# Optimization experiments

Hardware: AMD Instinct MI355X
Metric: run time of the kernel (lower is better)

## Reference

```python
import jax, jax.numpy as jnp
import numpy as np

HEADS = 8

def setup_inputs() -> dict:
    key = jax.random.key(0)
    k1, k2, k3, k4 = jax.random.split(key, 4)
    B, C_IN, H, W = 16, 256, 64, 64
    C_OUT = 256
    s = 1.0 / np.sqrt(C_IN)
    x = jax.random.normal(k1, (B, C_IN, H, W), dtype=jnp.float32)
    wq = jax.random.normal(k2, (C_OUT, C_IN), dtype=jnp.float32) * s
    wk = jax.random.normal(k3, (C_OUT, C_IN), dtype=jnp.float32) * s
    wv = jax.random.normal(k4, (C_OUT, C_IN), dtype=jnp.float32) * s
    return {"x": x, "wq": wq, "wk": wk, "wv": wv}

def _feat(t):
    # ELU(x) + 1  (positive feature map for linear attention)
    return jax.nn.elu(t) + 1.0

def reference(x, wq, wk, wv):
    B, C, H, W = x.shape
    M = H * W
    c_out = wq.shape[0]
    dh = c_out // HEADS
    scale = 1.0 / np.sqrt(dh)
    xf = x.reshape(B, C, M)  # flatten spatial
    # 1x1 conv (no bias) == channel matmul; reshape to [B, heads, dh, M]
    def proj(w):
        return jnp.einsum('oc,bcm->bom', w, xf).reshape(B, HEADS, dh, M)
    q = _feat(proj(wq)) * scale
    k = _feat(proj(wk)) * scale
    v = proj(wv)
    # linear attention: KV = k v^T over spatial, then apply to q
    KV = jnp.einsum('bhcm,bhdm->bhcd', k, v)          # [B,h,dh,dh]
    out = jnp.einsum('bhcd,bhcm->bhdm', KV, q)        # [B,h,dh,M]
    k_sum = k.sum(axis=-1)                             # [B,h,dh]
    denom = jnp.einsum('bhcm,bhc->bhm', q, k_sum)      # [B,h,M]
    denom = jnp.maximum(denom, 1e-6)[:, :, None, :]
    out = out / denom
    return out.reshape(B, c_out, H, W)
```

## Files before the change

### kernel.cpp

```cpp
#include <hip/hip_runtime.h>
#include <hip/hip_bf16.h>


typedef __attribute__((ext_vector_type(8))) short bf16x8;
typedef __attribute__((ext_vector_type(4))) float f32x4;
typedef __attribute__((ext_vector_type(4))) unsigned int u32x4;
typedef __attribute__((ext_vector_type(4))) float float4v;

#define DEVI static __device__ __forceinline__

DEVI unsigned short f2bf(float f){
  unsigned int u = __builtin_bit_cast(unsigned int, f);
  u = (u + 0x7fffu + ((u >> 16) & 1u)) >> 16;
  return (unsigned short)u;
}
DEVI unsigned int pk2(float a, float b){
  return (unsigned int)f2bf(a) | ((unsigned int)f2bf(b) << 16);
}
DEVI float feat(float p){
  return (p > 0.f ? p + 1.f : __expf(p)) * 0.17677669529663687f;
}

DEVI f32x4 mfma16(u32x4 a, u32x4 b, f32x4 c){
  return __builtin_amdgcn_mfma_f32_16x16x32_bf16(
      __builtin_bit_cast(bf16x8, a), __builtin_bit_cast(bf16x8, b), c, 0, 0, 0);
}

DEVI int swz8(int m){ return ((m ^ (m >> 3)) & 7) << 4; }

typedef __attribute__((address_space(3))) unsigned int as3_u32;
typedef __attribute__((address_space(1))) const unsigned int as1_u32;
DEVI void gload16(const void* g, void* l){
  __builtin_amdgcn_global_load_lds((as1_u32*)g, (as3_u32*)l, 16, 0, 0);
}
DEVI void stage_tile(const char* src, void* buf, int w, int lane){
  #pragma unroll
  for (int i = 0; i < 4; ++i){
    int ub = w * 1024 + i * 8192;
    gload16(src + ub + lane * 16, (char*)buf + ub);
  }
}

DEVI void stage_load(const float* __restrict__ xb, int m0, int tid, float4v* r){
  #pragma unroll
  for (int it = 0; it < 2; ++it){
    int cq = (tid >> 4) + it * 32;
    int mq = tid & 15;
    const float* p = xb + (size_t)(cq * 4) * 4096 + m0 + mq * 4;
    r[it*4+0] = *(const float4v*)(p);
    r[it*4+1] = *(const float4v*)(p + 4096);
    r[it*4+2] = *(const float4v*)(p + 8192);
    r[it*4+3] = *(const float4v*)(p + 12288);
  }
}
DEVI void stage_write(unsigned short* xT, int tid, const float4v* r){
  #pragma unroll
  for (int it = 0; it < 2; ++it){
    int cq = (tid >> 4) + it * 32;
    int mq = tid & 15;
    int c0 = cq * 4, ml0 = mq * 4;
    #pragma unroll
    for (int j = 0; j < 4; ++j){
      int m = ml0 + j;
      unsigned int lo = pk2(r[it*4+0][j], r[it*4+1][j]);
      unsigned int hi = pk2(r[it*4+2][j], r[it*4+3][j]);
      int off = m * 512 + ((c0 * 2) ^ swz8(m));
      unsigned long long v = (unsigned long long)lo | ((unsigned long long)hi << 32);
      *(unsigned long long*)((char*)xT + off) = v;
    }
  }
}

__global__ void wconv(const float* __restrict__ wq, const float* __restrict__ wk,
                      const float* __restrict__ wv,
                      unsigned short* __restrict__ wkvf, unsigned short* __restrict__ wqf){
  int t = blockIdx.x * 256 + threadIdx.x;
  if (t < 16384){
    int lane = t & 63, kk = (t >> 6) & 7, ot = (t >> 9) & 3, h = t >> 11;
    int l15 = lane & 15, hi = lane >> 4;
    const float* src = (ot < 2) ? (wk + (size_t)(h * 32 + ot * 16 + l15) * 256)
                                : (wv + (size_t)(h * 32 + (ot - 2) * 16 + l15) * 256);
    src += kk * 32 + hi * 8;
    unsigned short* dst = wkvf + (size_t)t * 8;
    #pragma unroll
    for (int j = 0; j < 8; ++j) dst[j] = f2bf(src[j]);
  } else if (t < 24576){
    int u = t - 16384;
    int lane = u & 63, kk = (u >> 6) & 7, ot = (u >> 9) & 1, h = u >> 10;
    int l15 = lane & 15, hi = lane >> 4;
    const float* src = wq + (size_t)(h * 32 + ot * 16 + l15) * 256 + kk * 32 + hi * 8;
    unsigned short* dst = wqf + (size_t)u * 8;
    #pragma unroll
    for (int j = 0; j < 8; ++j) dst[j] = f2bf(src[j]);
  }
}

__global__ void __launch_bounds__(512) xcvt(const float* __restrict__ x,
                                            unsigned short* __restrict__ ximg){
  __shared__ __align__(16) unsigned short xT[16384];
  const int tid = threadIdx.x;
  const int ch = blockIdx.x, b = blockIdx.y;
  const float* xb = x + (size_t)b * (256 * 4096);
  for (int sub = 0; sub < 2; ++sub){
    int m0 = ch * 128 + sub * 64;
    float4v rs[8];
    stage_load(xb, m0, tid, rs);
    if (sub) __syncthreads();
    stage_write(xT, tid, rs);
    __syncthreads();
    unsigned short* dst = ximg + ((size_t)b * 64 + (m0 >> 6)) * 16384;
    #pragma unroll
    for (int i = 0; i < 4; ++i){
      u32x4 v = *(const u32x4*)((const char*)xT + tid * 16 + i * 8192);
      *(u32x4*)((char*)dst + tid * 16 + i * 8192) = v;
    }
  }
}

DEVI void compute_sub(const unsigned short* __restrict__ xT,
                      const unsigned short* __restrict__ wkvf,
                      int w, int l15, int hi, int lane,
                      f32x4 (&kvacc)[2][2], f32x4 (&ksacc)[2], u32x4 ones){
  f32x4 acc[4][4];
  #pragma unroll
  for (int a1 = 0; a1 < 4; ++a1)
    #pragma unroll
    for (int a2 = 0; a2 < 4; ++a2) acc[a1][a2] = f32x4{0.f,0.f,0.f,0.f};

  for (int kk = 0; kk < 8; ++kk){
    u32x4 xf[4];
    #pragma unroll
    for (int nt = 0; nt < 4; ++nt){
      int m = nt * 16 + l15;
      xf[nt] = *(const u32x4*)((const char*)xT + m * 512 + ((kk * 64 + hi * 16) ^ swz8(m)));
    }
    #pragma unroll
    for (int ot = 0; ot < 4; ++ot){
      u32x4 wf = *(const u32x4*)(wkvf + ((((size_t)w * 4 + ot) * 8 + kk) * 64 + lane) * 8);
      #pragma unroll
      for (int nt = 0; nt < 4; ++nt) acc[nt][ot] = mfma16(xf[nt], wf, acc[nt][ot]);
    }
  }
  #pragma unroll
  for (int g = 0; g < 2; ++g){
    u32x4 kf[2], vf[2];
    #pragma unroll
    for (int t2 = 0; t2 < 2; ++t2){
      kf[t2][0] = pk2(feat(acc[2*g][t2][0]),   feat(acc[2*g][t2][1]));
      kf[t2][1] = pk2(feat(acc[2*g][t2][2]),   feat(acc[2*g][t2][3]));
      kf[t2][2] = pk2(feat(acc[2*g+1][t2][0]), feat(acc[2*g+1][t2][1]));
      kf[t2][3] = pk2(feat(acc[2*g+1][t2][2]), feat(acc[2*g+1][t2][3]));
      vf[t2][0] = pk2(acc[2*g][t2+2][0],   acc[2*g][t2+2][1]);
      vf[t2][1] = pk2(acc[2*g][t2+2][2],   acc[2*g][t2+2][3]);
      vf[t2][2] = pk2(acc[2*g+1][t2+2][0], acc[2*g+1][t2+2][1]);
      vf[t2][3] = pk2(acc[2*g+1][t2+2][2], acc[2*g+1][t2+2][3]);
    }
    #pragma unroll
    for (int ct = 0; ct < 2; ++ct){
      #pragma unroll
      for (int dt = 0; dt < 2; ++dt)
        kvacc[ct][dt] = mfma16(kf[ct], vf[dt], kvacc[ct][dt]);
      ksacc[ct] = mfma16(kf[ct], ones, ksacc[ct]);
    }
  }
}

__global__ void __launch_bounds__(512) k_kv(const unsigned short* __restrict__ ximg,
        const unsigned short* __restrict__ wkvf,
        float* __restrict__ kvp, float* __restrict__ ksp){
  __shared__ __align__(16) unsigned short xT[2][16384];
  const int tid = threadIdx.x, lane = tid & 63, w = tid >> 6;
  const int l15 = lane & 15, hi = lane >> 4;
  const int ch = blockIdx.x, b = blockIdx.y;
  const char* src = (const char*)(ximg + ((size_t)b * 64 + ch * 2) * 16384);

  f32x4 kvacc[2][2];
  f32x4 ksacc[2];
  #pragma unroll
  for (int i = 0; i < 2; ++i){
    ksacc[i] = f32x4{0.f,0.f,0.f,0.f};
    #pragma unroll
    for (int j = 0; j < 2; ++j) kvacc[i][j] = f32x4{0.f,0.f,0.f,0.f};
  }
  u32x4 ones = {0u,0u,0u,0u};
  if (l15 == 0){ ones[0] = ones[1] = ones[2] = ones[3] = 0x3f803f80u; }

  stage_tile(src, xT[0], w, lane);
  __syncthreads();
  stage_tile(src + 32768, xT[1], w, lane);
  compute_sub(xT[0], wkvf, w, l15, hi, lane, kvacc, ksacc, ones);
  __syncthreads();
  compute_sub(xT[1], wkvf, w, l15, hi, lane, kvacc, ksacc, ones);

  size_t base = (((size_t)b * 32 + ch) * 8 + w) * 1024;
  #pragma unroll
  for (int ct = 0; ct < 2; ++ct){
    #pragma unroll
    for (int dt = 0; dt < 2; ++dt){
      #pragma unroll
      for (int r = 0; r < 4; ++r){
        int c = ct * 16 + hi * 4 + r, d = dt * 16 + l15;
        kvp[base + c * 32 + d] = kvacc[ct][dt][r];
      }
    }
  }
  if (l15 == 0){
    size_t kb = (((size_t)b * 32 + ch) * 8 + w) * 32;
    #pragma unroll
    for (int ct = 0; ct < 2; ++ct)
      #pragma unroll
      for (int r = 0; r < 4; ++r) ksp[kb + ct * 16 + hi * 4 + r] = ksacc[ct][r];
  }
}

__global__ void k_red(const float* __restrict__ kvp, const float* __restrict__ ksp,
                      unsigned short* __restrict__ kvt, unsigned short* __restrict__ ksb){
  int t = blockIdx.x * 256 + threadIdx.x;
  int dq = t & 7;
  int c  = (t >> 3) & 31;
  int h  = (t >> 8) & 7;
  int b  = t >> 11;
  float4v s = {0.f,0.f,0.f,0.f};
  for (int c2 = 0; c2 < 32; ++c2){
    const float* p = kvp + ((((size_t)b * 32 + c2) * 8 + h) * 1024) + c * 32 + dq * 4;
    float4v r = *(const float4v*)p;
    s.x += r.x; s.y += r.y; s.z += r.z; s.w += r.w;
  }
  int pos = ((c >> 2) & 3) * 8 + ((c >> 4) << 2) + (c & 3);
  unsigned short* q = kvt + ((size_t)b * 8 + h) * 1024;
  q[(dq * 4 + 0) * 32 + pos] = f2bf(s.x);
  q[(dq * 4 + 1) * 32 + pos] = f2bf(s.y);
  q[(dq * 4 + 2) * 32 + pos] = f2bf(s.z);
  q[(dq * 4 + 3) * 32 + pos] = f2bf(s.w);
  if (dq == 0){
    float ks = 0.f;
    for (int c2 = 0; c2 < 32; ++c2)
      ks += ksp[(((size_t)b * 32 + c2) * 8 + h) * 32 + c];
    ksb[((size_t)b * 8 + h) * 32 + pos] = f2bf(ks);
  }
}

DEVI void q_sub(const unsigned short* __restrict__ xT,
                const unsigned short* __restrict__ wqf,
                u32x4 afkv0, u32x4 afkv1, u32x4 afd,
                int w, int l15, int hi, int lane, float* __restrict__ ob){
  f32x4 qa[2][4];
  #pragma unroll
  for (int a1 = 0; a1 < 2; ++a1)
    #pragma unroll
    for (int a2 = 0; a2 < 4; ++a2) qa[a1][a2] = f32x4{0.f,0.f,0.f,0.f};

  for (int kk = 0; kk < 8; ++kk){
    u32x4 xf[4];
    #pragma unroll
    for (int nt = 0; nt < 4; ++nt){
      int m = nt * 16 + l15;
      xf[nt] = *(const u32x4*)((const char*)xT + m * 512 + ((kk * 64 + hi * 16) ^ swz8(m)));
    }
    #pragma unroll
    for (int ot = 0; ot < 2; ++ot){
      u32x4 wf = *(const u32x4*)(wqf + ((((size_t)w * 2 + ot) * 8 + kk) * 64 + lane) * 8);
      #pragma unroll
      for (int nt = 0; nt < 4; ++nt) qa[ot][nt] = mfma16(wf, xf[nt], qa[ot][nt]);
    }
  }

  #pragma unroll
  for (int nt = 0; nt < 4; ++nt){
    u32x4 bq;
    bq[0] = pk2(feat(qa[0][nt][0]), feat(qa[0][nt][1]));
    bq[1] = pk2(feat(qa[0][nt][2]), feat(qa[0][nt][3]));
    bq[2] = pk2(feat(qa[1][nt][0]), feat(qa[1][nt][1]));
    bq[3] = pk2(feat(qa[1][nt][2]), feat(qa[1][nt][3]));

    f32x4 o0 = {0.f,0.f,0.f,0.f}, o1 = {0.f,0.f,0.f,0.f}, dn = {0.f,0.f,0.f,0.f};
    o0 = mfma16(afkv0, bq, o0);
    o1 = mfma16(afkv1, bq, o1);
    dn = mfma16(afd, bq, dn);
    float dv = __shfl(dn[0], l15, 64);
    float inv = 1.0f / fmaxf(dv, 1e-6f);
    #pragma unroll
    for (int r = 0; r < 4; ++r){
      ob[(size_t)(hi * 4 + r) * 4096 + nt * 16 + l15]      = o0[r] * inv;
      ob[(size_t)(16 + hi * 4 + r) * 4096 + nt * 16 + l15] = o1[r] * inv;
    }
  }
}

__global__ void __launch_bounds__(512) k_q(const unsigned short* __restrict__ ximg,
        const unsigned short* __restrict__ wqf,
        const unsigned short* __restrict__ kvt,
        const unsigned short* __restrict__ ksb,
        float* __restrict__ out){
  __shared__ __align__(16) unsigned short xT[2][16384];
  const int tid = threadIdx.x, lane = tid & 63, w = tid >> 6;
  const int l15 = lane & 15, hi = lane >> 4;
  const int ch = blockIdx.x, b = blockIdx.y;
  const char* src = (const char*)(ximg + ((size_t)b * 64 + ch * 2) * 16384);

  size_t kvbase = ((size_t)b * 8 + w) * 1024;
  u32x4 afkv0 = *(const u32x4*)(kvt + kvbase + (size_t)l15 * 32 + hi * 8);
  u32x4 afkv1 = *(const u32x4*)(kvt + kvbase + (size_t)(16 + l15) * 32 + hi * 8);
  u32x4 afd = {0u,0u,0u,0u};
  if (l15 == 0) afd = *(const u32x4*)(ksb + ((size_t)b * 8 + w) * 32 + hi * 8);

  stage_tile(src, xT[0], w, lane);
  __syncthreads();
  stage_tile(src + 32768, xT[1], w, lane);

  float* ob = out + ((size_t)b * 256 + w * 32) * 4096 + ch * 128;
  q_sub(xT[0], wqf, afkv0, afkv1, afd, w, l15, hi, lane, ob);
  __syncthreads();
  q_sub(xT[1], wqf, afkv0, afkv1, afd, w, l15, hi, lane, ob + 64);
}

extern "C" void kernel_launch(void* const* d_in, const int* in_sizes, int n_in,
                              void* d_out, int out_size, void* d_ws, size_t ws_size,
                              hipStream_t stream) {
  const float* x  = (const float*)d_in[0];
  const float* wq = (const float*)d_in[1];
  const float* wk = (const float*)d_in[2];
  const float* wv = (const float*)d_in[3];
  float* out = (float*)d_out;
  char* ws = (char*)d_ws;

  unsigned short* wkvf = (unsigned short*)(ws);
  unsigned short* wqf  = (unsigned short*)(ws + 262144);
  unsigned short* kvt  = (unsigned short*)(ws + 393216);
  unsigned short* ksb  = (unsigned short*)(ws + 655360);
  float* kvp = (float*)(ws + 1048576);
  float* ksp = (float*)(ws + 17825792);
  unsigned short* ximg = (unsigned short*)(ws + 18350080);

  hipLaunchKernelGGL(wconv, dim3(96), dim3(256), 0, stream, wq, wk, wv, wkvf, wqf);
  hipLaunchKernelGGL(xcvt,  dim3(32, 16), dim3(512), 0, stream, x, ximg);
  hipLaunchKernelGGL(k_kv,  dim3(32, 16), dim3(512), 0, stream, ximg, wkvf, kvp, ksp);
  hipLaunchKernelGGL(k_red, dim3(128), dim3(256), 0, stream, kvp, ksp, kvt, ksb);
  hipLaunchKernelGGL(k_q,   dim3(32, 16), dim3(512), 0, stream, ximg, wqf, kvt, ksb, out);
}
```

Baseline: 85.74 us.

## Fuse fp32-to-bf16 x conversion into KV kernel and drop separate xcvt pass

Removes the standalone xcvt kernel and has k_kv load fp32 x directly, convert it to bf16 into swizzled LDS, compute the KV partials, and write the bf16 image out for the later q kernel. This avoids one kernel launch and a full read of the bf16 image back from memory. The second sub-tile's global load overlaps compute of the first. In exchange, k_kv carries the conversion work and extra register pressure from holding the staged floats.

```diff
diff --git a/kernel.cpp b/kernel.cpp
--- a/kernel.cpp
+++ b/kernel.cpp
@@ -68,6 +68,13 @@
       unsigned long long v = (unsigned long long)lo | ((unsigned long long)hi << 32);
       *(unsigned long long*)((char*)xT + off) = v;
     }
+  }
+}
+DEVI void dump_tile(const unsigned short* xT, unsigned short* dst, int tid){
+  #pragma unroll
+  for (int i = 0; i < 4; ++i){
+    u32x4 v = *(const u32x4*)((const char*)xT + tid * 16 + i * 8192);
+    *(u32x4*)((char*)dst + tid * 16 + i * 8192) = v;
   }
 }
 
@@ -95,28 +102,6 @@
   }
 }
 
-__global__ void __launch_bounds__(512) xcvt(const float* __restrict__ x,
-                                            unsigned short* __restrict__ ximg){
-  __shared__ __align__(16) unsigned short xT[16384];
-  const int tid = threadIdx.x;
-  const int ch = blockIdx.x, b = blockIdx.y;
-  const float* xb = x + (size_t)b * (256 * 4096);
-  for (int sub = 0; sub < 2; ++sub){
-    int m0 = ch * 128 + sub * 64;
-    float4v rs[8];
-    stage_load(xb, m0, tid, rs);
-    if (sub) __syncthreads();
-    stage_write(xT, tid, rs);
-    __syncthreads();
-    unsigned short* dst = ximg + ((size_t)b * 64 + (m0 >> 6)) * 16384;
-    #pragma unroll
-    for (int i = 0; i < 4; ++i){
-      u32x4 v = *(const u32x4*)((const char*)xT + tid * 16 + i * 8192);
-      *(u32x4*)((char*)dst + tid * 16 + i * 8192) = v;
-    }
-  }
-}
-
 DEVI void compute_sub(const unsigned short* __restrict__ xT,
                       const unsigned short* __restrict__ wkvf,
                       int w, int l15, int hi, int lane,
@@ -165,14 +150,16 @@
   }
 }
 
-__global__ void __launch_bounds__(512) k_kv(const unsigned short* __restrict__ ximg,
+__global__ void __launch_bounds__(512) k_kv(const float* __restrict__ x,
         const unsigned short* __restrict__ wkvf,
-        float* __restrict__ kvp, float* __restrict__ ksp){
+        float* __restrict__ kvp, float* __restrict__ ksp,
+        unsigned short* __restrict__ ximg){
   __shared__ __align__(16) unsigned short xT[2][16384];
   const int tid = threadIdx.x, lane = tid & 63, w = tid >> 6;
   const int l15 = lane & 15, hi = lane >> 4;
   const int ch = blockIdx.x, b = blockIdx.y;
-  const char* src = (const char*)(ximg + ((size_t)b * 64 + ch * 2) * 16384);
+  const float* xb = x + (size_t)b * (256 * 4096);
+  unsigned short* img = ximg + ((size_t)b * 64 + ch * 2) * 16384;
 
   f32x4 kvacc[2][2];
   f32x4 ksacc[2];
@@ -185,12 +172,17 @@
   u32x4 ones = {0u,0u,0u,0u};
   if (l15 == 0){ ones[0] = ones[1] = ones[2] = ones[3] = 0x3f803f80u; }
 
-  stage_tile(src, xT[0], w, lane);
+  float4v rs[8];
+  stage_load(xb, ch * 128, tid, rs);
+  stage_write(xT[0], tid, rs);
   __syncthreads();
-  stage_tile(src + 32768, xT[1], w, lane);
+  stage_load(xb, ch * 128 + 64, tid, rs);
   compute_sub(xT[0], wkvf, w, l15, hi, lane, kvacc, ksacc, ones);
+  dump_tile(xT[0], img, tid);
+  stage_write(xT[1], tid, rs);
   __syncthreads();
   compute_sub(xT[1], wkvf, w, l15, hi, lane, kvacc, ksacc, ones);
+  dump_tile(xT[1], img + 16384, tid);
 
   size_t base = (((size_t)b * 32 + ch) * 8 + w) * 1024;
   #pragma unroll
@@ -333,8 +325,7 @@
   unsigned short* ximg = (unsigned short*)(ws + 18350080);
 
   hipLaunchKernelGGL(wconv, dim3(96), dim3(256), 0, stream, wq, wk, wv, wkvf, wqf);
-  hipLaunchKernelGGL(xcvt,  dim3(32, 16), dim3(512), 0, stream, x, ximg);
-  hipLaunchKernelGGL(k_kv,  dim3(32, 16), dim3(512), 0, stream, ximg, wkvf, kvp, ksp);
+  hipLaunchKernelGGL(k_kv,  dim3(32, 16), dim3(512), 0, stream, x, wkvf, kvp, ksp, ximg);
   hipLaunchKernelGGL(k_red, dim3(128), dim3(256), 0, stream, kvp, ksp, kvt, ksb);
   hipLaunchKernelGGL(k_q,   dim3(32, 16), dim3(512), 0, stream, ximg, wqf, kvt, ksb, out);
 }
```

New measurement: 81.04 us. 5.5% less time.

## Pre-swizzle bf16 x image into MFMA fragment order and drop LDS staging

Applied to the files above, without the earlier changes.

The conversion kernel now writes the bf16 x tile directly in MFMA-fragment order, so each lane's 16-byte fragment is contiguous in global memory. The KV and Q kernels then load fragments straight from global memory and skip the async global-to-LDS staging, the shared buffers and the barriers. The kk loops are also fully unrolled. In exchange, all 8 waves in a block re-read the same x fragments from global memory or cache instead of sharing one LDS copy. The loads are also no longer overlapped through the double-buffered LDS prefetch.

```diff
diff --git a/kernel.cpp b/kernel.cpp
--- a/kernel.cpp
+++ b/kernel.cpp
@@ -27,19 +27,6 @@
 }
 
 DEVI int swz8(int m){ return ((m ^ (m >> 3)) & 7) << 4; }
-
-typedef __attribute__((address_space(3))) unsigned int as3_u32;
-typedef __attribute__((address_space(1))) const unsigned int as1_u32;
-DEVI void gload16(const void* g, void* l){
-  __builtin_amdgcn_global_load_lds((as1_u32*)g, (as3_u32*)l, 16, 0, 0);
-}
-DEVI void stage_tile(const char* src, void* buf, int w, int lane){
-  #pragma unroll
-  for (int i = 0; i < 4; ++i){
-    int ub = w * 1024 + i * 8192;
-    gload16(src + ub + lane * 16, (char*)buf + ub);
-  }
-}
 
 DEVI void stage_load(const float* __restrict__ xb, int m0, int tid, float4v* r){
   #pragma unroll
@@ -111,15 +98,19 @@
     unsigned short* dst = ximg + ((size_t)b * 64 + (m0 >> 6)) * 16384;
     #pragma unroll
     for (int i = 0; i < 4; ++i){
-      u32x4 v = *(const u32x4*)((const char*)xT + tid * 16 + i * 8192);
-      *(u32x4*)((char*)dst + tid * 16 + i * 8192) = v;
-    }
-  }
-}
-
-DEVI void compute_sub(const unsigned short* __restrict__ xT,
+      int f = i * 512 + tid;
+      int lane = f & 63, nt = (f >> 6) & 3, kk = f >> 8;
+      int m = nt * 16 + (lane & 15);
+      int col = (kk * 64 + (lane >> 4) * 16) ^ swz8(m);
+      u32x4 v = *(const u32x4*)((const char*)xT + m * 512 + col);
+      *(u32x4*)((char*)dst + (size_t)f * 16) = v;
+    }
+  }
+}
+
+DEVI void compute_sub(const unsigned short* __restrict__ tile,
                       const unsigned short* __restrict__ wkvf,
-                      int w, int l15, int hi, int lane,
+                      int w, int lane,
                       f32x4 (&kvacc)[2][2], f32x4 (&ksacc)[2], u32x4 ones){
   f32x4 acc[4][4];
   #pragma unroll
@@ -127,13 +118,12 @@
     #pragma unroll
     for (int a2 = 0; a2 < 4; ++a2) acc[a1][a2] = f32x4{0.f,0.f,0.f,0.f};
 
+  #pragma unroll
   for (int kk = 0; kk < 8; ++kk){
     u32x4 xf[4];
     #pragma unroll
-    for (int nt = 0; nt < 4; ++nt){
-      int m = nt * 16 + l15;
-      xf[nt] = *(const u32x4*)((const char*)xT + m * 512 + ((kk * 64 + hi * 16) ^ swz8(m)));
-    }
+    for (int nt = 0; nt < 4; ++nt)
+      xf[nt] = *(const u32x4*)(tile + (((size_t)kk * 4 + nt) * 64 + lane) * 8);
     #pragma unroll
     for (int ot = 0; ot < 4; ++ot){
       u32x4 wf = *(const u32x4*)(wkvf + ((((size_t)w * 4 + ot) * 8 + kk) * 64 + lane) * 8);
@@ -168,11 +158,10 @@
 __global__ void __launch_bounds__(512) k_kv(const unsigned short* __restrict__ ximg,
         const unsigned short* __restrict__ wkvf,
         float* __restrict__ kvp, float* __restrict__ ksp){
-  __shared__ __align__(16) unsigned short xT[2][16384];
   const int tid = threadIdx.x, lane = tid & 63, w = tid >> 6;
   const int l15 = lane & 15, hi = lane >> 4;
   const int ch = blockIdx.x, b = blockIdx.y;
-  const char* src = (const char*)(ximg + ((size_t)b * 64 + ch * 2) * 16384);
+  const unsigned short* tile = ximg + ((size_t)b * 64 + ch * 2) * 16384;
 
   f32x4 kvacc[2][2];
   f32x4 ksacc[2];
@@ -185,12 +174,8 @@
   u32x4 ones = {0u,0u,0u,0u};
   if (l15 == 0){ ones[0] = ones[1] = ones[2] = ones[3] = 0x3f803f80u; }
 
-  stage_tile(src, xT[0], w, lane);
-  __syncthreads();
-  stage_tile(src + 32768, xT[1], w, lane);
-  compute_sub(xT[0], wkvf, w, l15, hi, lane, kvacc, ksacc, ones);
-  __syncthreads();
-  compute_sub(xT[1], wkvf, w, l15, hi, lane, kvacc, ksacc, ones);
+  compute_sub(tile,         wkvf, w, lane, kvacc, ksacc, ones);
+  compute_sub(tile + 16384, wkvf, w, lane, kvacc, ksacc, ones);
 
   size_t base = (((size_t)b * 32 + ch) * 8 + w) * 1024;
   #pragma unroll
@@ -240,7 +225,7 @@
   }
 }
 
-DEVI void q_sub(const unsigned short* __restrict__ xT,
+DEVI void q_sub(const unsigned short* __restrict__ tile,
                 const unsigned short* __restrict__ wqf,
                 u32x4 afkv0, u32x4 afkv1, u32x4 afd,
                 int w, int l15, int hi, int lane, float* __restrict__ ob){
@@ -250,13 +235,12 @@
     #pragma unroll
     for (int a2 = 0; a2 < 4; ++a2) qa[a1][a2] = f32x4{0.f,0.f,0.f,0.f};
 
+  #pragma unroll
   for (int kk = 0; kk < 8; ++kk){
     u32x4 xf[4];
     #pragma unroll
-    for (int nt = 0; nt < 4; ++nt){
-      int m = nt * 16 + l15;
-      xf[nt] = *(const u32x4*)((const char*)xT + m * 512 + ((kk * 64 + hi * 16) ^ swz8(m)));
-    }
+    for (int nt = 0; nt < 4; ++nt)
+      xf[nt] = *(const u32x4*)(tile + (((size_t)kk * 4 + nt) * 64 + lane) * 8);
     #pragma unroll
     for (int ot = 0; ot < 2; ++ot){
       u32x4 wf = *(const u32x4*)(wqf + ((((size_t)w * 2 + ot) * 8 + kk) * 64 + lane) * 8);
@@ -292,11 +276,10 @@
         const unsigned short* __restrict__ kvt,
         const unsigned short* __restrict__ ksb,
         float* __restrict__ out){
-  __shared__ __align__(16) unsigned short xT[2][16384];
   const int tid = threadIdx.x, lane = tid & 63, w = tid >> 6;
   const int l15 = lane & 15, hi = lane >> 4;
   const int ch = blockIdx.x, b = blockIdx.y;
-  const char* src = (const char*)(ximg + ((size_t)b * 64 + ch * 2) * 16384);
+  const unsigned short* tile = ximg + ((size_t)b * 64 + ch * 2) * 16384;
 
   size_t kvbase = ((size_t)b * 8 + w) * 1024;
   u32x4 afkv0 = *(const u32x4*)(kvt + kvbase + (size_t)l15 * 32 + hi * 8);
@@ -304,14 +287,9 @@
   u32x4 afd = {0u,0u,0u,0u};
   if (l15 == 0) afd = *(const u32x4*)(ksb + ((size_t)b * 8 + w) * 32 + hi * 8);
 
-  stage_tile(src, xT[0], w, lane);
-  __syncthreads();
-  stage_tile(src + 32768, xT[1], w, lane);
-
   float* ob = out + ((size_t)b * 256 + w * 32) * 4096 + ch * 128;
-  q_sub(xT[0], wqf, afkv0, afkv1, afd, w, l15, hi, lane, ob);
-  __syncthreads();
-  q_sub(xT[1], wqf, afkv0, afkv1, afd, w, l15, hi, lane, ob + 64);
+  q_sub(tile,         wqf, afkv0, afkv1, afd, w, l15, hi, lane, ob);
+  q_sub(tile + 16384, wqf, afkv0, afkv1, afd, w, l15, hi, lane, ob + 64);
 }
 
 extern "C" void kernel_launch(void* const* d_in, const int* in_sizes, int n_in,
```

Result: slower. 89.80 us (+4.7%).
